# Kernel tuning notes

Hardware: AMD Instinct MI355X
Metric: run time of the kernel (lower is better)

## Reference

```python
import jax, jax.numpy as jnp
import numpy as np

H = 8
D_MODEL = 1024
DIM_G = 64
WAVE_LEN = 1000.0


def box_relational_embedding(f_g):
    # f_g: [B, N, 4] -> [B, N, N, 64] trigonometric geometry embedding
    B, N, _ = f_g.shape
    x_min, y_min, x_max, y_max = jnp.split(f_g, 4, axis=-1)  # each [B, N, 1]
    cx = (x_min + x_max) * 0.5
    cy = (y_min + y_max) * 0.5
    w = x_max - x_min + 1.0
    h = y_max - y_min + 1.0
    # row i vs column j deltas, normalized by row box size
    dx = jnp.log(jnp.maximum(jnp.abs((cx - cx.reshape(B, 1, N)) / w), 1e-3))
    dy = jnp.log(jnp.maximum(jnp.abs((cy - cy.reshape(B, 1, N)) / h), 1e-3))
    dw = jnp.log(w / w.reshape(B, 1, N))
    dh = jnp.log(h / h.reshape(B, 1, N))
    pos = jnp.stack([dx, dy, dw, dh], axis=-1)  # [B, N, N, 4]
    feat_range = jnp.arange(DIM_G // 8, dtype=jnp.float32) / (DIM_G / 8.0)
    dim_mat = 1.0 / jnp.power(WAVE_LEN, feat_range)  # [8]
    mul = (100.0 * pos)[..., None] * dim_mat  # [B, N, N, 4, 8]
    mul = mul.reshape(B, N, N, DIM_G // 2)
    return jnp.concatenate([jnp.sin(mul), jnp.cos(mul)], axis=-1)  # [B, N, N, 64]


def setup_inputs() -> dict:
    key = jax.random.key(0)
    ks = jax.random.split(key, 12)
    B, N, D = 16, 256, D_MODEL
    q = jax.random.normal(ks[0], (B, N, D), jnp.float32)
    k = jax.random.normal(ks[1], (B, N, D), jnp.float32)
    v = jax.random.normal(ks[2], (B, N, D), jnp.float32)
    # valid boxes: x_max > x_min, y_max > y_min
    xy = jax.random.uniform(ks[3], (B, N, 2), jnp.float32) * 100.0
    wh = jax.random.uniform(ks[4], (B, N, 2), jnp.float32) * 50.0 + 1.0
    input_box = jnp.concatenate([xy, xy + wh], axis=-1)  # [B, N, 4]
    s = 0.02
    Wq = jax.random.normal(ks[5], (D, D), jnp.float32) * s
    Wk = jax.random.normal(ks[6], (D, D), jnp.float32) * s
    Wv = jax.random.normal(ks[7], (D, D), jnp.float32) * s
    Wo = jax.random.normal(ks[8], (D, D), jnp.float32) * s
    bq = jnp.zeros((D,), jnp.float32)
    bk = jnp.zeros((D,), jnp.float32)
    bv = jnp.zeros((D,), jnp.float32)
    bo = jnp.zeros((D,), jnp.float32)
    Wg = jax.random.normal(ks[9], (H, DIM_G), jnp.float32) * 0.1  # stacked per-head Linear(64,1)
    bg = jax.random.normal(ks[10], (H,), jnp.float32) * 0.1
    return {"input_query": q, "input_key": k, "input_value": v, "input_box": input_box,
            "Wq": Wq, "bq": bq, "Wk": Wk, "bk": bk, "Wv": Wv, "bv": bv,
            "Wg": Wg, "bg": bg, "Wo": Wo, "bo": bo}


def reference(input_query, input_key, input_value, input_box,
              Wq, bq, Wk, bk, Wv, bv, Wg, bg, Wo, bo):
    B, N, D = input_query.shape
    d_k = D // H

    def proj(x, W, b):
        return (x @ W + b).reshape(B, N, H, d_k).transpose(0, 2, 1, 3)  # [B,H,N,dk]

    q = proj(input_query, Wq, bq)
    k = proj(input_key, Wk, bk)
    v = proj(input_value, Wv, bv)

    emb = box_relational_embedding(input_box)  # [B, N, N, 64]
    # per-head Linear(64 -> 1), stacked: [B, H, N, N]
    rel_w = jax.nn.relu(jnp.einsum('bmng,hg->bhmn', emb, Wg) + bg[None, :, None, None])

    scores = jnp.einsum('bhqd,bhkd->bhqk', q, k) / np.sqrt(d_k).astype(np.float32)
    logits = jnp.log(jnp.maximum(rel_w, 1e-6)) + scores
    attn = jax.nn.softmax(logits, axis=-1)  # [B, H, N, N]
    out = jnp.einsum('bhqk,bhkd->bhqd', attn, v)
    out = out.transpose(0, 2, 1, 3).reshape(B, N, D)
    return out @ Wo + bo
```

## Files before the change

### kernel.cpp

```cpp
#include <hip/hip_runtime.h>
#include <hip/hip_bf16.h>
#include <hip/hip_fp16.h>
#include <math.h>

#define B_  16
#define N_  256
#define D_  1024
#define H_  8
#define DK_ 128

typedef unsigned short u16;
typedef __attribute__((ext_vector_type(8))) short s8v;
typedef __attribute__((ext_vector_type(4))) float f4v;

__device__ __forceinline__ u16 f2b(float x) {
    union { float f; unsigned u; } v; v.f = x;
    unsigned r = v.u + 0x7fffu + ((v.u >> 16) & 1u);
    return (u16)(r >> 16);
}

__device__ __forceinline__ void gload16(void* lds, const void* g) {
    __builtin_amdgcn_global_load_lds(
        (const __attribute__((address_space(1))) void*)g,
        (__attribute__((address_space(3))) void*)lds, 16, 0, 0);
}

__global__ __launch_bounds__(256)
void cvt_kernel(const float* __restrict__ x0, const float* __restrict__ x1,
                const float* __restrict__ x2, u16* __restrict__ out)
{
    const float* in = (blockIdx.y == 0) ? x0 : (blockIdx.y == 1) ? x1 : x2;
    u16* o = out + (size_t)blockIdx.y * 4194304;
    const int i = blockIdx.x * 256 + threadIdx.x;
    const float4 a = ((const float4*)in)[2 * i];
    const float4 b = ((const float4*)in)[2 * i + 1];
    union { u16 s[8]; uint4 v; } t;
    t.s[0] = f2b(a.x); t.s[1] = f2b(a.y); t.s[2] = f2b(a.z); t.s[3] = f2b(a.w);
    t.s[4] = f2b(b.x); t.s[5] = f2b(b.y); t.s[6] = f2b(b.z); t.s[7] = f2b(b.w);
    ((uint4*)o)[i] = t.v;
}

__global__ __launch_bounds__(256)
void cvtT_kernel(const float* __restrict__ W0, const float* __restrict__ W1,
                 const float* __restrict__ W2, const float* __restrict__ W3,
                 u16* __restrict__ out)
{
    const float* W = (blockIdx.z == 0) ? W0 : (blockIdx.z == 1) ? W1 :
                     (blockIdx.z == 2) ? W2 : W3;
    u16* o = out + (size_t)blockIdx.z * (D_ * D_);
    __shared__ float t[32][33];
    const int k0 = blockIdx.x * 32, n0 = blockIdx.y * 32;
    const int c = threadIdx.x & 31, r8 = threadIdx.x >> 5;
#pragma unroll
    for (int rr = 0; rr < 4; ++rr)
        t[r8 + rr * 8][c] = W[(size_t)(k0 + r8 + rr * 8) * D_ + n0 + c];
    __syncthreads();
#pragma unroll
    for (int rr = 0; rr < 4; ++rr)
        o[(size_t)(n0 + r8 + rr * 8) * D_ + k0 + c] = f2b(t[c][r8 + rr * 8]);
}

__global__ __launch_bounds__(256)
void gemm_kernel(const u16* __restrict__ A0, const u16* __restrict__ Wt0,
                 const float* __restrict__ b0, const float* __restrict__ b1,
                 const float* __restrict__ b2, void* __restrict__ outb,
                 int mode)
{
    __shared__ __align__(16) u16 As[2][128][32];
    __shared__ __align__(16) u16 Bs[2][128][32];

    const int z = blockIdx.z;
    const u16* A  = A0  + (size_t)z * 4194304;
    const u16* Wt = Wt0 + (size_t)z * 1048576;
    const float* bias = (z == 0) ? b0 : (z == 1) ? b1 : b2;

    const int bid = blockIdx.x;
    const int xcd = bid & 7;
    const int wic = bid >> 3;
    const int by  = xcd * 4 + (wic & 3);
    const int bx  = wic >> 2;
    const int m0  = by * 128;
    const int n0  = bx * 128;

    const int tid  = threadIdx.x;
    const int lane = tid & 63;
    const int w    = tid >> 6;
    const int l15  = lane & 15;
    const int l4   = lane >> 4;
    const int wr   = w >> 1;
    const int wc   = w & 1;

    const int gr   = tid >> 2;
    const int c4   = tid & 3;
    const int sw   = (gr >> 1) & 3;
    const int scol = (c4 ^ sw) * 8;
    const int doff = c4 * 8;
    const u16* asrc = A  + (size_t)(m0 + gr) * 1024 + scol;
    const u16* bsrc = Wt + (size_t)(n0 + gr) * 1024 + scol;

    const int fc = (l4 ^ ((l15 >> 1) & 3)) * 8;

    f4v acc[4][4] = {};

#define STAGE(buf, kt) do { \
        const int k0_ = (kt) * 32; \
        gload16(&As[buf][gr][doff],      asrc + k0_); \
        gload16(&As[buf][gr + 64][doff], asrc + 64 * 1024 + k0_); \
        gload16(&Bs[buf][gr][doff],      bsrc + k0_); \
        gload16(&Bs[buf][gr + 64][doff], bsrc + 64 * 1024 + k0_); \
    } while (0)

    STAGE(0, 0);
    __syncthreads();

    for (int kt = 0; kt < 32; ++kt) {
        const int cur = kt & 1;
        if (kt < 31) STAGE(cur ^ 1, kt + 1);

        s8v af[4], bf[4];
#pragma unroll
        for (int i = 0; i < 4; ++i)
            af[i] = *(const s8v*)&As[cur][wr * 64 + i * 16 + l15][fc];
#pragma unroll
        for (int j = 0; j < 4; ++j)
            bf[j] = *(const s8v*)&Bs[cur][wc * 64 + j * 16 + l15][fc];
#pragma unroll
        for (int i = 0; i < 4; ++i)
#pragma unroll
            for (int j = 0; j < 4; ++j)
                acc[i][j] = __builtin_amdgcn_mfma_f32_16x16x32_bf16(
                    af[i], bf[j], acc[i][j], 0, 0, 0);

        __syncthreads();
    }
#undef STAGE

#pragma unroll
    for (int j = 0; j < 4; ++j) {
        const int n = n0 + wc * 64 + j * 16 + l15;
        const float bb = bias[n];
#pragma unroll
        for (int i = 0; i < 4; ++i) {
            const int mbase = m0 + wr * 64 + i * 16 + l4 * 4;
            if (mode == 0) {
#pragma unroll
                for (int reg = 0; reg < 4; ++reg)
                    ((float*)outb)[(size_t)(mbase + reg) * 1024 + n] =
                        acc[i][j][reg] + bb;
            } else if (z == 2) {
                const int b = mbase >> 8, tok = mbase & 255;
                const int h = n >> 7, d = n & 127;
                ushort4 st;
                st.x = f2b(acc[i][j][0] + bb);
                st.y = f2b(acc[i][j][1] + bb);
                st.z = f2b(acc[i][j][2] + bb);
                st.w = f2b(acc[i][j][3] + bb);
                *(ushort4*)&((u16*)outb)[(size_t)z * 4194304 +
                    (((size_t)b * H_ + h) * DK_ + d) * N_ + tok] = st;
            } else {
                const int h = n >> 7, d = n & 127;
#pragma unroll
                for (int reg = 0; reg < 4; ++reg) {
                    const int m = mbase + reg;
                    const int b = m >> 8, tok = m & 255;
                    ((u16*)outb)[(size_t)z * 4194304 +
                        (((size_t)b * H_ + h) * N_ + tok) * DK_ + d] =
                        f2b(acc[i][j][reg] + bb);
                }
            }
        }
    }
}

__global__ __launch_bounds__(256)
void boxbias_kernel(const float* __restrict__ fg, const float* __restrict__ Wg,
                    const float* __restrict__ bg, _Float16* __restrict__ lb)
{
    __shared__ float sWg[512];
    __shared__ float sbg[8];
    const int tid = threadIdx.x;
    const int b = blockIdx.x >> 8;
    const int i = blockIdx.x & 255;

    sWg[tid] = Wg[tid];
    sWg[tid + 256] = Wg[tid + 256];
    if (tid < 8) sbg[tid] = bg[tid];

    const float4 bi = *(const float4*)&fg[(size_t)(b * N_ + i) * 4];
    const float cxi = 0.5f * (bi.x + bi.z);
    const float cyi = 0.5f * (bi.y + bi.w);
    const float wi  = bi.z - bi.x + 1.0f;
    const float hi  = bi.w - bi.y + 1.0f;

    const int j = tid;
    const float4 bj = *(const float4*)&fg[(size_t)(b * N_ + j) * 4];
    const float cxj = 0.5f * (bj.x + bj.z);
    const float cyj = 0.5f * (bj.y + bj.w);
    const float wj  = bj.z - bj.x + 1.0f;
    const float hj  = bj.w - bj.y + 1.0f;

    const float pos[4] = {
        logf(fmaxf(fabsf((cxi - cxj) / wi), 1e-3f)) * 100.0f,
        logf(fmaxf(fabsf((cyi - cyj) / hi), 1e-3f)) * 100.0f,
        logf(wi / wj) * 100.0f,
        logf(hi / hj) * 100.0f
    };
    const float dim[8] = {1.0f, 0.421696503f, 0.177827941f, 0.0749894209f,
                          0.0316227766f, 0.0133352143f, 0.00562341325f, 0.00237137371f};

    float sv[32], cv[32];
#pragma unroll
    for (int p = 0; p < 4; ++p)
#pragma unroll
        for (int q = 0; q < 8; ++q)
            __sincosf(pos[p] * dim[q], &sv[p * 8 + q], &cv[p * 8 + q]);

    __syncthreads();
#pragma unroll
    for (int h = 0; h < 8; ++h) {
        float acc = sbg[h];
        const float* wrow = &sWg[h * 64];
#pragma unroll
        for (int g = 0; g < 32; ++g)
            acc = fmaf(sv[g], wrow[g], fmaf(cv[g], wrow[32 + g], acc));
        const float rel = fmaxf(acc, 0.0f);
        lb[(((size_t)b * H_ + h) * N_ + i) * N_ + j] =
            (_Float16)logf(fmaxf(rel, 1e-6f));
    }
}

__global__ __launch_bounds__(256)
void attn_mfma_kernel(const u16* __restrict__ qp, const u16* __restrict__ kp,
                      const u16* __restrict__ vp, const _Float16* __restrict__ lb,
                      u16* __restrict__ ao)
{
    __shared__ __align__(16) u16 Ks[32][136];
    __shared__ __align__(16) u16 Vt[128][40];
    __shared__ __align__(16) u16 Ps[4][32][40];

    const int tid  = threadIdx.x;
    const int lane = tid & 63;
    const int w    = tid >> 6;
    const int l15  = lane & 15;
    const int l4   = lane >> 4;
    const int bh   = blockIdx.x >> 1;
    const int qt   = blockIdx.x & 1;
    const int q0   = qt * 128 + w * 32;

    s8v qf[2][4];
    const u16* qb = qp + ((size_t)bh * N_ + q0) * DK_;
#pragma unroll
    for (int mf = 0; mf < 2; ++mf)
#pragma unroll
        for (int ks = 0; ks < 4; ++ks)
            qf[mf][ks] = *(const s8v*)(qb + (size_t)(mf * 16 + l15) * DK_ + ks * 32 + l4 * 8);

    f4v o[2][8] = {};
    float m_r[2][4], l_r[2][4];
#pragma unroll
    for (int mf = 0; mf < 2; ++mf)
#pragma unroll
        for (int r = 0; r < 4; ++r) { m_r[mf][r] = -INFINITY; l_r[mf][r] = 0.0f; }

    const float scale = 0.08838834764831845f;
    const _Float16* lbb = lb + ((size_t)bh * N_ + q0) * N_;

    const int sr = tid >> 3;
    const int sc = (tid & 7) * 16;
    const int vr = tid >> 2;
    const int vs = (tid & 3) * 8;

    for (int kt = 0; kt < 8; ++kt) {
        __syncthreads();
        {
            const u16* ksrc = kp + ((size_t)bh * N_ + kt * 32) * DK_;
            *(s8v*)&Ks[sr][sc]     = *(const s8v*)(ksrc + (size_t)sr * DK_ + sc);
            *(s8v*)&Ks[sr][sc + 8] = *(const s8v*)(ksrc + (size_t)sr * DK_ + sc + 8);
        }
        {
            const u16* vsrc = vp + ((size_t)bh * DK_ + vr) * N_ + kt * 32 + vs;
            const s8v v0 = *(const s8v*)vsrc;
            const s8v v1 = *(const s8v*)(vsrc + 64 * N_);
            *(s8v*)&Vt[vr][vs]      = v0;
            *(s8v*)&Vt[vr + 64][vs] = v1;
        }
        __syncthreads();

        f4v s[2][2] = {};
#pragma unroll
        for (int ks = 0; ks < 4; ++ks) {
#pragma unroll
            for (int kf = 0; kf < 2; ++kf) {
                const s8v kb = *(const s8v*)&Ks[kf * 16 + l15][ks * 32 + l4 * 8];
#pragma unroll
                for (int mf = 0; mf < 2; ++mf)
                    s[mf][kf] = __builtin_amdgcn_mfma_f32_16x16x32_bf16(
                        qf[mf][ks], kb, s[mf][kf], 0, 0, 0);
            }
        }
#pragma unroll
        for (int mf = 0; mf < 2; ++mf)
#pragma unroll
            for (int kf = 0; kf < 2; ++kf)
#pragma unroll
                for (int r = 0; r < 4; ++r)
                    s[mf][kf][r] = fmaf(s[mf][kf][r], scale, (float)
                        lbb[(size_t)(mf * 16 + l4 * 4 + r) * N_ + kt * 32 + kf * 16 + l15]);

#pragma unroll
        for (int mf = 0; mf < 2; ++mf) {
            float rm[4], al[4];
#pragma unroll
            for (int r = 0; r < 4; ++r) rm[r] = fmaxf(s[mf][0][r], s[mf][1][r]);
#pragma unroll
            for (int st = 1; st <= 8; st <<= 1)
#pragma unroll
                for (int r = 0; r < 4; ++r) rm[r] = fmaxf(rm[r], __shfl_xor(rm[r], st));
#pragma unroll
            for (int r = 0; r < 4; ++r) {
                const float mn = fmaxf(m_r[mf][r], rm[r]);
                al[r] = __expf(m_r[mf][r] - mn);
                m_r[mf][r] = mn;
            }
            float p0[4], p1[4], rs[4];
#pragma unroll
            for (int r = 0; r < 4; ++r) {
                p0[r] = __expf(s[mf][0][r] - m_r[mf][r]);
                p1[r] = __expf(s[mf][1][r] - m_r[mf][r]);
                rs[r] = p0[r] + p1[r];
            }
#pragma unroll
            for (int st = 1; st <= 8; st <<= 1)
#pragma unroll
                for (int r = 0; r < 4; ++r) rs[r] += __shfl_xor(rs[r], st);
#pragma unroll
            for (int r = 0; r < 4; ++r) {
                l_r[mf][r] = l_r[mf][r] * al[r] + rs[r];
                Ps[w][mf * 16 + l4 * 4 + r][l15]      = f2b(p0[r]);
                Ps[w][mf * 16 + l4 * 4 + r][16 + l15] = f2b(p1[r]);
            }
#pragma unroll
            for (int nf = 0; nf < 8; ++nf)
#pragma unroll
                for (int r = 0; r < 4; ++r) o[mf][nf][r] *= al[r];
        }

        s8v pa[2];
#pragma unroll
        for (int mf = 0; mf < 2; ++mf)
            pa[mf] = *(const s8v*)&Ps[w][mf * 16 + l15][l4 * 8];
#pragma unroll
        for (int nf = 0; nf < 8; ++nf) {
            const s8v vb = *(const s8v*)&Vt[nf * 16 + l15][l4 * 8];
#pragma unroll
            for (int mf = 0; mf < 2; ++mf)
                o[mf][nf] = __builtin_amdgcn_mfma_f32_16x16x32_bf16(
                    pa[mf], vb, o[mf][nf], 0, 0, 0);
        }
    }

    const int b = bh >> 3, h = bh & 7;
#pragma unroll
    for (int mf = 0; mf < 2; ++mf) {
        float inv[4];
#pragma unroll
        for (int r = 0; r < 4; ++r) inv[r] = 1.0f / l_r[mf][r];
#pragma unroll
        for (int nf = 0; nf < 8; ++nf) {
#pragma unroll
            for (int r = 0; r < 4; ++r) {
                const int tok = q0 + mf * 16 + l4 * 4 + r;
                const int d = nf * 16 + l15;
                ao[(((size_t)b * N_ + tok) * H_ + h) * DK_ + d] = f2b(o[mf][nf][r] * inv[r]);
            }
        }
    }
}

extern "C" void kernel_launch(void* const* d_in, const int* in_sizes, int n_in,
                              void* d_out, int out_size, void* d_ws, size_t ws_size,
                              hipStream_t stream)
{
    const float* xq = (const float*)d_in[0];
    const float* xk = (const float*)d_in[1];
    const float* xv = (const float*)d_in[2];
    const float* fg = (const float*)d_in[3];
    const float* Wq = (const float*)d_in[4];
    const float* bq = (const float*)d_in[5];
    const float* Wk = (const float*)d_in[6];
    const float* bk = (const float*)d_in[7];
    const float* Wv = (const float*)d_in[8];
    const float* bv = (const float*)d_in[9];
    const float* Wg = (const float*)d_in[10];
    const float* bg = (const float*)d_in[11];
    const float* Wo = (const float*)d_in[12];
    const float* bo = (const float*)d_in[13];

    char* w8 = (char*)d_ws;
    u16*      xb  = (u16*)(w8);
    u16*      Wt  = (u16*)(w8 + 25165824);
    u16*      qkv = (u16*)(w8 + 33554432);
    _Float16* lb  = (_Float16*)(w8 + 58720256);
    u16*      ao  = (u16*)(w8 + 75497472);

    cvt_kernel<<<dim3(2048, 3), 256, 0, stream>>>(xq, xk, xv, xb);
    cvtT_kernel<<<dim3(32, 32, 4), 256, 0, stream>>>(Wq, Wk, Wv, Wo, Wt);

    gemm_kernel<<<dim3(256, 1, 3), 256, 0, stream>>>(xb, Wt, bq, bk, bv, qkv, 1);

    boxbias_kernel<<<B_ * N_, 256, 0, stream>>>(fg, Wg, bg, lb);

    attn_mfma_kernel<<<B_ * H_ * 2, 256, 0, stream>>>(
        qkv, qkv + 4194304, qkv + 2 * 4194304, lb, ao);

    gemm_kernel<<<dim3(256, 1, 1), 256, 0, stream>>>(
        ao, Wt + 3 * 1048576, bo, bo, bo, d_out, 0);
}
```

Before: 138.7 us.

## Triple-buffer GEMM loads with explicit vmcnt waits and smaller output-projection tile

The GEMM kernel moves from a double-buffered LDS pipeline with __syncthreads to a three-stage ring that prefetches two k-tiles ahead and uses explicit s_waitcnt vmcnt counts plus raw barriers. The kernel is templated on tile height, fragment count, loads per stage and output mode, which turns the mode branch into a compile-time choice. The output projection now uses 64-row tiles, doubling its block count to 512 so more CUs are busy. Risks are the extra LDS per block and correctness depending on hand-tuned vmcnt counts that must match the number of outstanding loads.

```diff
diff --git a/kernel.cpp b/kernel.cpp
--- a/kernel.cpp
+++ b/kernel.cpp
@@ -24,6 +24,13 @@
         (const __attribute__((address_space(1))) void*)g,
         (__attribute__((address_space(3))) void*)lds, 16, 0, 0);
 }
+
+__device__ __forceinline__ void waitv8() { asm volatile("s_waitcnt vmcnt(8)" ::: "memory"); }
+__device__ __forceinline__ void waitv6() { asm volatile("s_waitcnt vmcnt(6)" ::: "memory"); }
+__device__ __forceinline__ void waitv4() { asm volatile("s_waitcnt vmcnt(4)" ::: "memory"); }
+__device__ __forceinline__ void waitv3() { asm volatile("s_waitcnt vmcnt(3)" ::: "memory"); }
+__device__ __forceinline__ void waitv0() { asm volatile("s_waitcnt vmcnt(0)" ::: "memory"); }
+__device__ __forceinline__ void membar() { asm volatile("" ::: "memory"); }
 
 __global__ __launch_bounds__(256)
 void cvt_kernel(const float* __restrict__ x0, const float* __restrict__ x1,
@@ -60,14 +67,16 @@
         o[(size_t)(n0 + r8 + rr * 8) * D_ + k0 + c] = f2b(t[c][r8 + rr * 8]);
 }
 
+template<int BM, int FM, int LOADS, int MODE>
 __global__ __launch_bounds__(256)
 void gemm_kernel(const u16* __restrict__ A0, const u16* __restrict__ Wt0,
                  const float* __restrict__ b0, const float* __restrict__ b1,
-                 const float* __restrict__ b2, void* __restrict__ outb,
-                 int mode)
-{
-    __shared__ __align__(16) u16 As[2][128][32];
-    __shared__ __align__(16) u16 Bs[2][128][32];
+                 const float* __restrict__ b2, void* __restrict__ outb)
+{
+    constexpr int WM  = FM * 16;
+    constexpr int MT8 = (4096 / BM) / 8;
+    __shared__ __align__(16) u16 As[3][BM][32];
+    __shared__ __align__(16) u16 Bs[3][128][32];
 
     const int z = blockIdx.z;
     const u16* A  = A0  + (size_t)z * 4194304;
@@ -77,9 +86,9 @@
     const int bid = blockIdx.x;
     const int xcd = bid & 7;
     const int wic = bid >> 3;
-    const int by  = xcd * 4 + (wic & 3);
-    const int bx  = wic >> 2;
-    const int m0  = by * 128;
+    const int by  = xcd * MT8 + (wic & (MT8 - 1));
+    const int bx  = wic / MT8;
+    const int m0  = by * BM;
     const int n0  = bx * 128;
 
     const int tid  = threadIdx.x;
@@ -92,80 +101,92 @@
 
     const int gr   = tid >> 2;
     const int c4   = tid & 3;
-    const int sw   = (gr >> 1) & 3;
-    const int scol = (c4 ^ sw) * 8;
+    const int scol = (c4 ^ ((gr >> 1) & 3)) * 8;
     const int doff = c4 * 8;
     const u16* asrc = A  + (size_t)(m0 + gr) * 1024 + scol;
     const u16* bsrc = Wt + (size_t)(n0 + gr) * 1024 + scol;
-
     const int fc = (l4 ^ ((l15 >> 1) & 3)) * 8;
 
-    f4v acc[4][4] = {};
-
-#define STAGE(buf, kt) do { \
-        const int k0_ = (kt) * 32; \
-        gload16(&As[buf][gr][doff],      asrc + k0_); \
-        gload16(&As[buf][gr + 64][doff], asrc + 64 * 1024 + k0_); \
-        gload16(&Bs[buf][gr][doff],      bsrc + k0_); \
-        gload16(&Bs[buf][gr + 64][doff], bsrc + 64 * 1024 + k0_); \
-    } while (0)
-
-    STAGE(0, 0);
-    __syncthreads();
+    auto stage = [&](int buf, int kt) {
+        const int k0_ = kt * 32;
+        gload16(&As[buf][gr][doff], asrc + k0_);
+        if constexpr (BM == 128)
+            gload16(&As[buf][gr + 64][doff], asrc + 64 * 1024 + k0_);
+        gload16(&Bs[buf][gr][doff], bsrc + k0_);
+        gload16(&Bs[buf][gr + 64][doff], bsrc + 64 * 1024 + k0_);
+    };
+
+    f4v acc[FM][4] = {};
+
+    stage(0, 0);
+    stage(1, 1);
+    int cur = 0, stg = 2;
 
     for (int kt = 0; kt < 32; ++kt) {
-        const int cur = kt & 1;
-        if (kt < 31) STAGE(cur ^ 1, kt + 1);
-
-        s8v af[4], bf[4];
-#pragma unroll
-        for (int i = 0; i < 4; ++i)
-            af[i] = *(const s8v*)&As[cur][wr * 64 + i * 16 + l15][fc];
+        membar();
+        __builtin_amdgcn_s_barrier();
+        if (kt < 30) {
+            stage(stg, kt + 2);
+            if constexpr (LOADS == 4) waitv8(); else waitv6();
+        } else if (kt == 30) {
+            if constexpr (LOADS == 4) waitv4(); else waitv3();
+        } else {
+            waitv0();
+        }
+        membar();
+        __builtin_amdgcn_s_barrier();
+
+        s8v af[FM], bf[4];
+#pragma unroll
+        for (int i = 0; i < FM; ++i)
+            af[i] = *(const s8v*)&As[cur][wr * WM + i * 16 + l15][fc];
 #pragma unroll
         for (int j = 0; j < 4; ++j)
             bf[j] = *(const s8v*)&Bs[cur][wc * 64 + j * 16 + l15][fc];
 #pragma unroll
-        for (int i = 0; i < 4; ++i)
+        for (int i = 0; i < FM; ++i)
 #pragma unroll
             for (int j = 0; j < 4; ++j)
                 acc[i][j] = __builtin_amdgcn_mfma_f32_16x16x32_bf16(
                     af[i], bf[j], acc[i][j], 0, 0, 0);
 
-        __syncthreads();
+        cur = (cur == 2) ? 0 : cur + 1;
+        stg = (stg == 2) ? 0 : stg + 1;
     }
-#undef STAGE
 
 #pragma unroll
     for (int j = 0; j < 4; ++j) {
         const int n = n0 + wc * 64 + j * 16 + l15;
         const float bb = bias[n];
 #pragma unroll
-        for (int i = 0; i < 4; ++i) {
-            const int mbase = m0 + wr * 64 + i * 16 + l4 * 4;
-            if (mode == 0) {
+        for (int i = 0; i < FM; ++i) {
+            const int mbase = m0 + wr * WM + i * 16 + l4 * 4;
+            if constexpr (MODE == 0) {
 #pragma unroll
                 for (int reg = 0; reg < 4; ++reg)
                     ((float*)outb)[(size_t)(mbase + reg) * 1024 + n] =
                         acc[i][j][reg] + bb;
-            } else if (z == 2) {
-                const int b = mbase >> 8, tok = mbase & 255;
-                const int h = n >> 7, d = n & 127;
-                ushort4 st;
-                st.x = f2b(acc[i][j][0] + bb);
-                st.y = f2b(acc[i][j][1] + bb);
-                st.z = f2b(acc[i][j][2] + bb);
-                st.w = f2b(acc[i][j][3] + bb);
-                *(ushort4*)&((u16*)outb)[(size_t)z * 4194304 +
-                    (((size_t)b * H_ + h) * DK_ + d) * N_ + tok] = st;
             } else {
-                const int h = n >> 7, d = n & 127;
-#pragma unroll
-                for (int reg = 0; reg < 4; ++reg) {
-                    const int m = mbase + reg;
-                    const int b = m >> 8, tok = m & 255;
-                    ((u16*)outb)[(size_t)z * 4194304 +
-                        (((size_t)b * H_ + h) * N_ + tok) * DK_ + d] =
-                        f2b(acc[i][j][reg] + bb);
+                if (z == 2) {
+                    const int b = mbase >> 8, tok = mbase & 255;
+                    const int h = n >> 7, d = n & 127;
+                    ushort4 st;
+                    st.x = f2b(acc[i][j][0] + bb);
+                    st.y = f2b(acc[i][j][1] + bb);
+                    st.z = f2b(acc[i][j][2] + bb);
+                    st.w = f2b(acc[i][j][3] + bb);
+                    *(ushort4*)&((u16*)outb)[(size_t)z * 4194304 +
+                        (((size_t)b * H_ + h) * DK_ + d) * N_ + tok] = st;
+                } else {
+                    const int h = n >> 7, d = n & 127;
+#pragma unroll
+                    for (int reg = 0; reg < 4; ++reg) {
+                        const int m = mbase + reg;
+                        const int b = m >> 8, tok = m & 255;
+                        ((u16*)outb)[(size_t)z * 4194304 +
+                            (((size_t)b * H_ + h) * N_ + tok) * DK_ + d] =
+                            f2b(acc[i][j][reg] + bb);
+                    }
                 }
             }
         }
@@ -406,13 +427,14 @@
     cvt_kernel<<<dim3(2048, 3), 256, 0, stream>>>(xq, xk, xv, xb);
     cvtT_kernel<<<dim3(32, 32, 4), 256, 0, stream>>>(Wq, Wk, Wv, Wo, Wt);
 
-    gemm_kernel<<<dim3(256, 1, 3), 256, 0, stream>>>(xb, Wt, bq, bk, bv, qkv, 1);
+    gemm_kernel<128, 4, 4, 1><<<dim3(256, 1, 3), 256, 0, stream>>>(
+        xb, Wt, bq, bk, bv, qkv);
 
     boxbias_kernel<<<B_ * N_, 256, 0, stream>>>(fg, Wg, bg, lb);
 
     attn_mfma_kernel<<<B_ * H_ * 2, 256, 0, stream>>>(
         qkv, qkv + 4194304, qkv + 2 * 4194304, lb, ao);
 
-    gemm_kernel<<<dim3(256, 1, 1), 256, 0, stream>>>(
-        ao, Wt + 3 * 1048576, bo, bo, bo, d_out, 0);
-}
+    gemm_kernel<64, 2, 3, 0><<<dim3(512, 1, 1), 256, 0, stream>>>(
+        ao, Wt + 3 * 1048576, bo, bo, bo, d_out);
+}
```

After: 128.3 us. 7.5% less time.

## Replace GEMM with 256x256-tile 8-wave kernel using split-phase LDS pipeline

Applied to the files above, without the earlier changes.

Replaces the 128x128-tile, 4-wave bf16 GEMM with a 256x256-tile, 512-thread kernel that uses 64-wide K steps and 128 KB of dynamic LDS. Staging is split into quarter-tile phases interleaved with MFMA work, using explicit vmcnt waits, raw barriers and setprio around the MFMA blocks. The goal is more operand reuse per LDS load and more overlap of global-to-LDS copies with compute. In exchange the grid shrinks to 64 blocks per GEMM, far fewer than the GPU's CUs, and the XCD-aware block mapping is dropped.

```diff
diff --git a/kernel.cpp b/kernel.cpp
--- a/kernel.cpp
+++ b/kernel.cpp
@@ -24,6 +24,10 @@
         (const __attribute__((address_space(1))) void*)g,
         (__attribute__((address_space(3))) void*)lds, 16, 0, 0);
 }
+
+#define WV_(n) asm volatile("s_waitcnt vmcnt(" #n ")" ::: "memory")
+#define WV(n)  WV_(n)
+#define MEMBAR() asm volatile("" ::: "memory")
 
 __global__ __launch_bounds__(256)
 void cvt_kernel(const float* __restrict__ x0, const float* __restrict__ x1,
@@ -60,14 +64,87 @@
         o[(size_t)(n0 + r8 + rr * 8) * D_ + k0 + c] = f2b(t[c][r8 + rr * 8]);
 }
 
-__global__ __launch_bounds__(256)
-void gemm_kernel(const u16* __restrict__ A0, const u16* __restrict__ Wt0,
-                 const float* __restrict__ b0, const float* __restrict__ b1,
-                 const float* __restrict__ b2, void* __restrict__ outb,
-                 int mode)
-{
-    __shared__ __align__(16) u16 As[2][128][32];
-    __shared__ __align__(16) u16 Bs[2][128][32];
+#define AOFF(s,mh) (((s)*2+(mh))*8192)
+#define BOFF(s,nh) (32768 + ((s)*2+(nh))*8192)
+
+#define STG_A(ns, mh, kn) do { \
+    gload16(&lds8[AOFF(ns,mh) + adst],        aS + (size_t)(m0 + (mh)*64) * 1024 + (kn)); \
+    gload16(&lds8[AOFF(ns,mh) + 4096 + adst], aS + (size_t)(m0 + 128 + (mh)*64) * 1024 + (kn)); \
+} while (0)
+
+#define STG_B(ns, nh, kn) do { \
+    gload16(&lds8[BOFF(ns,nh) + bdst],        bS + (size_t)(n0 + (nh)*32) * 1024 + (kn)); \
+    gload16(&lds8[BOFF(ns,nh) + 4096 + bdst], bS + (size_t)(n0 + 128 + (nh)*32) * 1024 + (kn)); \
+} while (0)
+
+#define TILE(S, W0, W1, W2, DOSTG, KN) do { \
+     \
+    WV(W0); __builtin_amdgcn_s_barrier(); \
+    _Pragma("unroll") \
+    for (int i = 0; i < 4; ++i) { \
+        af[i][0] = *(const s8v*)&lds8[AOFF(S,0) + ar + i * 1024 + o0]; \
+        af[i][1] = *(const s8v*)&lds8[AOFF(S,0) + ar + i * 1024 + o1]; } \
+    _Pragma("unroll") \
+    for (int j = 0; j < 2; ++j) { \
+        bf0[j][0] = *(const s8v*)&lds8[BOFF(S,0) + br + j * 1024 + o0]; \
+        bf0[j][1] = *(const s8v*)&lds8[BOFF(S,0) + br + j * 1024 + o1]; } \
+    if (DOSTG) { STG_A((S)^1, 0, KN); STG_B((S)^1, 0, KN); } \
+    __builtin_amdgcn_s_setprio(1); \
+    _Pragma("unroll") \
+    for (int i = 0; i < 4; ++i) \
+        _Pragma("unroll") \
+        for (int j = 0; j < 2; ++j) { \
+            acc[i][j] = __builtin_amdgcn_mfma_f32_16x16x32_bf16(af[i][0], bf0[j][0], acc[i][j], 0, 0, 0); \
+            acc[i][j] = __builtin_amdgcn_mfma_f32_16x16x32_bf16(af[i][1], bf0[j][1], acc[i][j], 0, 0, 0); } \
+    __builtin_amdgcn_s_setprio(0); \
+     \
+    WV(W1); __builtin_amdgcn_s_barrier(); \
+    _Pragma("unroll") \
+    for (int j = 0; j < 2; ++j) { \
+        bf1[j][0] = *(const s8v*)&lds8[BOFF(S,1) + br + j * 1024 + o0]; \
+        bf1[j][1] = *(const s8v*)&lds8[BOFF(S,1) + br + j * 1024 + o1]; } \
+    if (DOSTG) { STG_B((S)^1, 1, KN); } \
+    __builtin_amdgcn_s_setprio(1); \
+    _Pragma("unroll") \
+    for (int i = 0; i < 4; ++i) \
+        _Pragma("unroll") \
+        for (int j = 0; j < 2; ++j) { \
+            acc[i][2+j] = __builtin_amdgcn_mfma_f32_16x16x32_bf16(af[i][0], bf1[j][0], acc[i][2+j], 0, 0, 0); \
+            acc[i][2+j] = __builtin_amdgcn_mfma_f32_16x16x32_bf16(af[i][1], bf1[j][1], acc[i][2+j], 0, 0, 0); } \
+    __builtin_amdgcn_s_setprio(0); \
+     \
+    WV(W2); __builtin_amdgcn_s_barrier(); \
+    _Pragma("unroll") \
+    for (int i = 0; i < 4; ++i) { \
+        af[i][0] = *(const s8v*)&lds8[AOFF(S,1) + ar + i * 1024 + o0]; \
+        af[i][1] = *(const s8v*)&lds8[AOFF(S,1) + ar + i * 1024 + o1]; } \
+    if (DOSTG) { STG_A((S)^1, 1, KN); } \
+    __builtin_amdgcn_s_setprio(1); \
+    _Pragma("unroll") \
+    for (int i = 0; i < 4; ++i) \
+        _Pragma("unroll") \
+        for (int j = 0; j < 2; ++j) { \
+            acc[4+i][2+j] = __builtin_amdgcn_mfma_f32_16x16x32_bf16(af[i][0], bf1[j][0], acc[4+i][2+j], 0, 0, 0); \
+            acc[4+i][2+j] = __builtin_amdgcn_mfma_f32_16x16x32_bf16(af[i][1], bf1[j][1], acc[4+i][2+j], 0, 0, 0); } \
+    __builtin_amdgcn_s_setprio(0); \
+     \
+    __builtin_amdgcn_s_setprio(1); \
+    _Pragma("unroll") \
+    for (int i = 0; i < 4; ++i) \
+        _Pragma("unroll") \
+        for (int j = 0; j < 2; ++j) { \
+            acc[4+i][j] = __builtin_amdgcn_mfma_f32_16x16x32_bf16(af[i][0], bf0[j][0], acc[4+i][j], 0, 0, 0); \
+            acc[4+i][j] = __builtin_amdgcn_mfma_f32_16x16x32_bf16(af[i][1], bf0[j][1], acc[4+i][j], 0, 0, 0); } \
+    __builtin_amdgcn_s_setprio(0); \
+} while (0)
+
+template<int MODE>
+__global__ __launch_bounds__(512, 2)
+void gemm8(const u16* __restrict__ A0, const u16* __restrict__ Wt0,
+           const float* __restrict__ b0, const float* __restrict__ b1,
+           const float* __restrict__ b2, void* __restrict__ outb)
+{
+    extern __shared__ u16 lds8[];
 
     const int z = blockIdx.z;
     const u16* A  = A0  + (size_t)z * 4194304;
@@ -75,86 +152,67 @@
     const float* bias = (z == 0) ? b0 : (z == 1) ? b1 : b2;
 
     const int bid = blockIdx.x;
-    const int xcd = bid & 7;
-    const int wic = bid >> 3;
-    const int by  = xcd * 4 + (wic & 3);
-    const int bx  = wic >> 2;
-    const int m0  = by * 128;
-    const int n0  = bx * 128;
+    const int m0  = (bid & 15) * 256;
+    const int n0  = (bid >> 4) * 256;
 
     const int tid  = threadIdx.x;
     const int lane = tid & 63;
     const int w    = tid >> 6;
     const int l15  = lane & 15;
     const int l4   = lane >> 4;
-    const int wr   = w >> 1;
-    const int wc   = w & 1;
-
-    const int gr   = tid >> 2;
-    const int c4   = tid & 3;
-    const int sw   = (gr >> 1) & 3;
-    const int scol = (c4 ^ sw) * 8;
-    const int doff = c4 * 8;
-    const u16* asrc = A  + (size_t)(m0 + gr) * 1024 + scol;
-    const u16* bsrc = Wt + (size_t)(n0 + gr) * 1024 + scol;
-
-    const int fc = (l4 ^ ((l15 >> 1) & 3)) * 8;
-
-    f4v acc[4][4] = {};
-
-#define STAGE(buf, kt) do { \
-        const int k0_ = (kt) * 32; \
-        gload16(&As[buf][gr][doff],      asrc + k0_); \
-        gload16(&As[buf][gr + 64][doff], asrc + 64 * 1024 + k0_); \
-        gload16(&Bs[buf][gr][doff],      bsrc + k0_); \
-        gload16(&Bs[buf][gr + 64][doff], bsrc + 64 * 1024 + k0_); \
-    } while (0)
-
-    STAGE(0, 0);
-    __syncthreads();
-
-    for (int kt = 0; kt < 32; ++kt) {
-        const int cur = kt & 1;
-        if (kt < 31) STAGE(cur ^ 1, kt + 1);
-
-        s8v af[4], bf[4];
-#pragma unroll
-        for (int i = 0; i < 4; ++i)
-            af[i] = *(const s8v*)&As[cur][wr * 64 + i * 16 + l15][fc];
-#pragma unroll
-        for (int j = 0; j < 4; ++j)
-            bf[j] = *(const s8v*)&Bs[cur][wc * 64 + j * 16 + l15][fc];
-#pragma unroll
-        for (int i = 0; i < 4; ++i)
-#pragma unroll
-            for (int j = 0; j < 4; ++j)
-                acc[i][j] = __builtin_amdgcn_mfma_f32_16x16x32_bf16(
-                    af[i], bf[j], acc[i][j], 0, 0, 0);
-
-        __syncthreads();
+    const int wr   = w >> 2;
+    const int wc   = w & 3;
+
+    const int ar = wr * 4096 + l15 * 64;
+    const int br = wc * 2048 + l15 * 64;
+    const int o0 = (l4 ^ (l15 & 7)) * 8;
+    const int o1 = o0 ^ 32;
+
+    const int rA   = tid >> 3;
+    const int cswz = ((tid & 7) ^ (rA & 7)) * 8;
+    const u16* aS  = A  + (size_t)rA * 1024 + cswz;
+    const u16* bS  = Wt + (size_t)((tid >> 8) * 64 + (rA & 31)) * 1024 + cswz;
+    const int adst = rA * 64 + (tid & 7) * 8;
+    const int bdst = (tid >> 8) * 2048 + (rA & 31) * 64 + (tid & 7) * 8;
+
+    f4v acc[8][4] = {};
+    s8v af[4][2], bf0[2][2], bf1[2][2];
+
+    STG_A(0, 0, 0); STG_B(0, 0, 0); MEMBAR();
+    STG_B(0, 1, 0); MEMBAR();
+    STG_A(0, 1, 0); MEMBAR();
+
+#pragma unroll 1
+    for (int tt = 0; tt < 14; tt += 2) {
+        TILE(0, 4, 6, 6, true, (tt + 1) * 64);
+        TILE(1, 4, 6, 6, true, (tt + 2) * 64);
     }
-#undef STAGE
-
-#pragma unroll
-    for (int j = 0; j < 4; ++j) {
-        const int n = n0 + wc * 64 + j * 16 + l15;
+    TILE(0, 4, 6, 6, true, 15 * 64);
+    TILE(1, 4, 2, 0, false, 0);
+
+#pragma unroll
+    for (int mh = 0; mh < 2; ++mh)
+#pragma unroll
+    for (int i = 0; i < 4; ++i)
+#pragma unroll
+    for (int nh = 0; nh < 2; ++nh)
+#pragma unroll
+    for (int j = 0; j < 2; ++j) {
+        const int n = n0 + wc * 64 + nh * 32 + j * 16 + l15;
         const float bb = bias[n];
-#pragma unroll
-        for (int i = 0; i < 4; ++i) {
-            const int mbase = m0 + wr * 64 + i * 16 + l4 * 4;
-            if (mode == 0) {
-#pragma unroll
-                for (int reg = 0; reg < 4; ++reg)
-                    ((float*)outb)[(size_t)(mbase + reg) * 1024 + n] =
-                        acc[i][j][reg] + bb;
-            } else if (z == 2) {
+        const int mbase = m0 + wr * 128 + mh * 64 + i * 16 + l4 * 4;
+        const f4v a = acc[mh * 4 + i][nh * 2 + j];
+        if constexpr (MODE == 0) {
+#pragma unroll
+            for (int reg = 0; reg < 4; ++reg)
+                ((float*)outb)[(size_t)(mbase + reg) * 1024 + n] = a[reg] + bb;
+        } else {
+            if (z == 2) {
                 const int b = mbase >> 8, tok = mbase & 255;
                 const int h = n >> 7, d = n & 127;
                 ushort4 st;
-                st.x = f2b(acc[i][j][0] + bb);
-                st.y = f2b(acc[i][j][1] + bb);
-                st.z = f2b(acc[i][j][2] + bb);
-                st.w = f2b(acc[i][j][3] + bb);
+                st.x = f2b(a[0] + bb); st.y = f2b(a[1] + bb);
+                st.z = f2b(a[2] + bb); st.w = f2b(a[3] + bb);
                 *(ushort4*)&((u16*)outb)[(size_t)z * 4194304 +
                     (((size_t)b * H_ + h) * DK_ + d) * N_ + tok] = st;
             } else {
@@ -164,8 +222,7 @@
                     const int m = mbase + reg;
                     const int b = m >> 8, tok = m & 255;
                     ((u16*)outb)[(size_t)z * 4194304 +
-                        (((size_t)b * H_ + h) * N_ + tok) * DK_ + d] =
-                        f2b(acc[i][j][reg] + bb);
+                        (((size_t)b * H_ + h) * N_ + tok) * DK_ + d] = f2b(a[reg] + bb);
                 }
             }
         }
@@ -403,16 +460,21 @@
     _Float16* lb  = (_Float16*)(w8 + 58720256);
     u16*      ao  = (u16*)(w8 + 75497472);
 
+    (void)hipFuncSetAttribute(reinterpret_cast<const void*>(&gemm8<1>),
+                              hipFuncAttributeMaxDynamicSharedMemorySize, 131072);
+    (void)hipFuncSetAttribute(reinterpret_cast<const void*>(&gemm8<0>),
+                              hipFuncAttributeMaxDynamicSharedMemorySize, 131072);
+
     cvt_kernel<<<dim3(2048, 3), 256, 0, stream>>>(xq, xk, xv, xb);
     cvtT_kernel<<<dim3(32, 32, 4), 256, 0, stream>>>(Wq, Wk, Wv, Wo, Wt);
 
-    gemm_kernel<<<dim3(256, 1, 3), 256, 0, stream>>>(xb, Wt, bq, bk, bv, qkv, 1);
+    gemm8<1><<<dim3(64, 1, 3), 512, 131072, stream>>>(xb, Wt, bq, bk, bv, qkv);
 
     boxbias_kernel<<<B_ * N_, 256, 0, stream>>>(fg, Wg, bg, lb);
 
     attn_mfma_kernel<<<B_ * H_ * 2, 256, 0, stream>>>(
         qkv, qkv + 4194304, qkv + 2 * 4194304, lb, ao);
 
-    gemm_kernel<<<dim3(256, 1, 1), 256, 0, stream>>>(
-        ao, Wt + 3 * 1048576, bo, bo, bo, d_out, 0);
-}
+    gemm8<0><<<dim3(64, 1, 1), 512, 131072, stream>>>(
+        ao, Wt + 3 * 1048576, bo, bo, bo, d_out);
+}
```

Result: faster. 133.7 us (-3.6%).
